# Performance work log

Measured on AMD Instinct MI355X. Metric: run time of the kernel, lower is better.

Reference implementation:

```python
import jax, jax.numpy as jnp
import numpy as np

B, SEQ, S, DIM_IN, DIM_K, DIM_V = 4, 2048, 128, 512, 64, 64
L = SEQ + 2 * S
NEG = -1e30  # stand-in for log(0) in the tril mask (finite for stable vjp)


def _layernorm(x, g, b, eps=1e-5):
    m = jnp.mean(x, axis=-1, keepdims=True)
    v = jnp.var(x, axis=-1, keepdims=True)
    return (x - m) / jnp.sqrt(v + eps) * g + b


def setup_inputs() -> dict:
    key = jax.random.key(0)
    ks = jax.random.split(key, 18)
    w = lambda k, shape, s=0.02: (jax.random.normal(k, shape, jnp.float32) * s)
    inp = {
        "x": jax.random.normal(ks[0], (B, L, DIM_IN), jnp.float32),
        "Wq": w(ks[1], (DIM_IN, DIM_K)),
        "Wk": w(ks[2], (DIM_IN, DIM_K)),
        "Wv": w(ks[3], (DIM_IN, DIM_V)),
        "Wq_s": w(ks[4], (DIM_IN, DIM_K)),
        "Wk_s": w(ks[5], (DIM_IN, DIM_K)),
        "Wv_s": w(ks[6], (DIM_IN, DIM_V)),
        "Wq_e": w(ks[7], (DIM_IN, DIM_K)),
        "Wk_e": w(ks[8], (DIM_IN, DIM_K)),
        "Wv_e": w(ks[9], (DIM_IN, DIM_V)),
        "ln_g": jnp.ones((DIM_IN,), jnp.float32),
        "ln_b": jnp.zeros((DIM_IN,), jnp.float32),
        "ln_s_g": jnp.ones((DIM_IN,), jnp.float32),
        "ln_s_b": jnp.zeros((DIM_IN,), jnp.float32),
        "ln_e_g": jnp.ones((DIM_IN,), jnp.float32),
        "ln_e_b": jnp.zeros((DIM_IN,), jnp.float32),
        "cope_emb": jax.random.normal(ks[10], (DIM_K, S), jnp.float32),
        "offset": 0,
    }
    return inp


def reference(x, Wq, Wk, Wv, Wq_s, Wk_s, Wv_s, Wq_e, Wk_e, Wv_e,
              ln_g, ln_b, ln_s_g, ln_s_b, ln_e_g, ln_e_b, cope_emb, offset):
    # extract_state: first/last state_len tokens
    xs, xm, xe = x[:, :S], x[:, S:L - S], x[:, -S:]
    xm = _layernorm(xm, ln_g, ln_b)
    xs = _layernorm(xs, ln_s_g, ln_s_b)
    xe = _layernorm(xe, ln_e_g, ln_e_b)

    q, k, v = xm @ Wq, xm @ Wk, xm @ Wv          # (B, SEQ, dk/dv)
    q_s, k_s, v_s = xs @ Wq_s, xs @ Wk_s, xs @ Wv_s
    q_e, k_e, v_e = xe @ Wq_e, xe @ Wk_e, xe @ Wv_e

    # CoPE bias over the non-state block
    logits = jnp.einsum('bqd,bkd->bqk', q, k)    # (B, SEQ, SEQ)
    gates = jax.nn.sigmoid(logits)
    pos = jnp.flip(jnp.cumsum(jnp.flip(gates, -1), axis=-1), -1)
    pos = jnp.minimum(pos, jnp.float32(S - 1))
    pos_ceil = jnp.ceil(pos).astype(jnp.int32)
    pos_floor = jnp.floor(pos).astype(jnp.int32)
    logits_int = jnp.einsum('bqd,dk->bqk', q, cope_emb)  # (B, SEQ, S)
    logits_c = jnp.take_along_axis(logits_int, pos_ceil, axis=-1)
    logits_f = jnp.take_along_axis(logits_int, pos_floor, axis=-1)
    wfrac = pos - pos_floor.astype(pos.dtype)
    bias = logits_c * wfrac + logits_f * (1.0 - wfrac)   # (B, SEQ, SEQ)

    q_full = jnp.concatenate([q_s, q, q_e], axis=1)      # (B, L, dk)
    k_full = jnp.concatenate([k_s, k, k_e], axis=1)
    v_full = jnp.concatenate([v_s, v, v_e], axis=1)

    # explicit tril log-mask bias with CoPE injected in the middle block
    tri = jnp.tril(jnp.ones((L, L), dtype=bool))
    attn_bias = jnp.where(tri, 0.0, NEG).astype(jnp.float32)
    attn_bias = jnp.broadcast_to(attn_bias, (B, L, L))
    attn_bias = attn_bias.at[:, S:L - S, S:L - S].add(bias)

    scale = 1.0 / jnp.sqrt(jnp.float32(DIM_K))
    scores = jnp.einsum('bqd,bkd->bqk', q_full, k_full) * scale + attn_bias
    att = jax.nn.softmax(scores, axis=-1)
    return jnp.einsum('bqk,bkd->bqd', att, v_full)       # (B, L, dv)
```

## Files before the change

kernel.cpp:

```cpp
#include <hip/hip_runtime.h>
#include <math.h>

#define B_    4
#define SEQ_  2048
#define S_    128
#define L_    2304
#define DIN   512
#define DK    64
#define NEGINF (-1e30f)
#define SCALE 0.125f
#define NCOLS 2176
#define NMID  8192
#define NEDGE 1024
#define LE    2304

typedef _Float16 f16;
typedef __attribute__((ext_vector_type(8))) _Float16 half8;
typedef __attribute__((ext_vector_type(4))) float f32x4;

union U4 { uint4 u; f16 h[8]; };

__global__ __launch_bounds__(256) void k_wsplit(
    const float* __restrict__ Wq,  const float* __restrict__ Wk,  const float* __restrict__ Wv,
    const float* __restrict__ Wqs, const float* __restrict__ Wks, const float* __restrict__ Wvs,
    const float* __restrict__ Wqe, const float* __restrict__ Wke, const float* __restrict__ Wve,
    f16* __restrict__ Wsp)
{
    __shared__ float xs[64 * 68];
    const int kt  = blockIdx.x;
    const int mat = blockIdx.y;
    const float* W;
    switch (mat) {
        case 0: W = Wq;  break; case 1: W = Wk;  break; case 2: W = Wv;  break;
        case 3: W = Wqs; break; case 4: W = Wks; break; case 5: W = Wvs; break;
        case 6: W = Wqe; break; case 7: W = Wke; break; default: W = Wve; break;
    }
    const int tid = threadIdx.x;
    const int k0  = kt * 64;
    #pragma unroll
    for (int i = 0; i < 4; ++i) {
        int g = tid + 256 * i;
        int k = g >> 4, c4 = g & 15;
        *(float4*)(xs + k * 68 + c4 * 4) = ((const float4*)W)[(size_t)(k0 + k) * 16 + c4];
    }
    __syncthreads();
    const int col = tid & 63, hf = tid >> 6;
    const int kk0 = hf * 16;
    U4 hi0, hi1, lo0, lo1;
    #pragma unroll
    for (int j = 0; j < 8; ++j) {
        float v0 = xs[(kk0 + j) * 68 + col];
        float v1 = xs[(kk0 + 8 + j) * 68 + col];
        hi0.h[j] = (f16)v0; lo0.h[j] = (f16)(v0 - (float)hi0.h[j]);
        hi1.h[j] = (f16)v1; lo1.h[j] = (f16)(v1 - (float)hi1.h[j]);
    }
    f16* dst = Wsp + (size_t)mat * 65536 + (size_t)col * 1024 + k0 + kk0;
    *(uint4*)(dst)       = hi0.u;
    *(uint4*)(dst + 8)   = hi1.u;
    *(uint4*)(dst + 512) = lo0.u;
    *(uint4*)(dst + 520) = lo1.u;
}

__global__ __launch_bounds__(256) void k_proj(
    const float* __restrict__ x, const f16* __restrict__ Wsp,
    const float* __restrict__ g0, const float* __restrict__ b0,
    const float* __restrict__ gs, const float* __restrict__ bs,
    const float* __restrict__ ge, const float* __restrict__ be,
    f16* __restrict__ qsp, f16* __restrict__ ksp, f16* __restrict__ vhT)
{
    __shared__ f16 As[32 * 136];
    __shared__ f16 Bs[3 * 64 * 136];
    __shared__ float mean_s[32], rstd_s[32];
    const int tid  = threadIdx.x;
    const int row0 = blockIdx.x * 32;
    const int rseq = row0 % L_;
    const int seg  = (rseq < S_) ? 0 : (rseq >= L_ - S_) ? 2 : 1;
    const int mat0 = (seg == 0) ? 3 : (seg == 2) ? 6 : 0;
    const float* gg = (seg == 0) ? gs : (seg == 2) ? ge : g0;
    const float* bb = (seg == 0) ? bs : (seg == 2) ? be : b0;

    {
        const int rr = tid >> 3, qq = tid & 7;
        const float4* xr = (const float4*)(x + (size_t)(row0 + rr) * DIN) + qq * 16;
        float s = 0.f, s2 = 0.f;
        #pragma unroll
        for (int i = 0; i < 16; ++i) {
            float4 v = xr[i];
            s  += v.x + v.y + v.z + v.w;
            s2 += v.x * v.x + v.y * v.y + v.z * v.z + v.w * v.w;
        }
        s  += __shfl_xor(s, 1);  s  += __shfl_xor(s, 2);  s  += __shfl_xor(s, 4);
        s2 += __shfl_xor(s2, 1); s2 += __shfl_xor(s2, 2); s2 += __shfl_xor(s2, 4);
        if (qq == 0) {
            float mean = s * (1.f / DIN);
            mean_s[rr] = mean;
            rstd_s[rr] = rsqrtf(s2 * (1.f / DIN) - mean * mean + 1e-5f);
        }
    }

    const int w = tid >> 6, lane = tid & 63;
    const int cl = lane & 15, quad = lane >> 4;
    const int r0 = 16 * (w >> 1), c0 = 32 * (w & 1);

    f32x4 acc[3][2];
    #pragma unroll
    for (int m = 0; m < 3; ++m)
        #pragma unroll
        for (int j = 0; j < 2; ++j) acc[m][j] = 0.f;

    for (int kc = 0; kc < DIN; kc += 64) {
        __syncthreads();
        {
            int r = tid >> 3, c8 = tid & 7;
            const float* xp = x + (size_t)(row0 + r) * DIN + kc + c8 * 8;
            float4 a0 = *(const float4*)xp;
            float4 a1 = *(const float4*)(xp + 4);
            float4 gA = *(const float4*)(gg + kc + c8 * 8);
            float4 gB = *(const float4*)(gg + kc + c8 * 8 + 4);
            float4 bA = *(const float4*)(bb + kc + c8 * 8);
            float4 bB = *(const float4*)(bb + kc + c8 * 8 + 4);
            float mean = mean_s[r], rstd = rstd_s[r];
            float n[8];
            n[0] = (a0.x - mean) * rstd * gA.x + bA.x;
            n[1] = (a0.y - mean) * rstd * gA.y + bA.y;
            n[2] = (a0.z - mean) * rstd * gA.z + bA.z;
            n[3] = (a0.w - mean) * rstd * gA.w + bA.w;
            n[4] = (a1.x - mean) * rstd * gB.x + bB.x;
            n[5] = (a1.y - mean) * rstd * gB.y + bB.y;
            n[6] = (a1.z - mean) * rstd * gB.z + bB.z;
            n[7] = (a1.w - mean) * rstd * gB.w + bB.w;
            U4 hi, lo;
            #pragma unroll
            for (int j = 0; j < 8; ++j) {
                hi.h[j] = (f16)n[j];
                lo.h[j] = (f16)(n[j] - (float)hi.h[j]);
            }
            *(uint4*)(As + r * 136 + c8 * 8)      = hi.u;
            *(uint4*)(As + r * 136 + 64 + c8 * 8) = lo.u;
        }
        #pragma unroll
        for (int i = 0; i < 6; ++i) {
            int g = tid + 256 * i;
            int mm = g >> 9, rem = g & 511;
            int col = rem >> 3, c8 = rem & 7;
            const f16* src = Wsp + (size_t)(mat0 + mm) * 65536 + (size_t)col * 1024 + kc + c8 * 8;
            f16* dst = Bs + mm * 8704 + col * 136 + c8 * 8;
            *(uint4*)(dst)      = *(const uint4*)(src);
            *(uint4*)(dst + 64) = *(const uint4*)(src + 512);
        }
        __syncthreads();
        #pragma unroll
        for (int h = 0; h < 2; ++h) {
            half8 ah, al;
            {
                const f16* base = As + (r0 + cl) * 136 + h * 32 + quad * 8;
                ah = *(const half8*)(base);
                al = *(const half8*)(base + 64);
            }
            #pragma unroll
            for (int m = 0; m < 3; ++m)
                #pragma unroll
                for (int cs = 0; cs < 2; ++cs) {
                    const f16* base = Bs + m * 8704 + (c0 + 16 * cs + cl) * 136 + h * 32 + quad * 8;
                    half8 bh = *(const half8*)(base);
                    half8 bl = *(const half8*)(base + 64);
                    acc[m][cs] = __builtin_amdgcn_mfma_f32_16x16x32_f16(ah, bh, acc[m][cs], 0, 0, 0);
                    acc[m][cs] = __builtin_amdgcn_mfma_f32_16x16x32_f16(ah, bl, acc[m][cs], 0, 0, 0);
                    acc[m][cs] = __builtin_amdgcn_mfma_f32_16x16x32_f16(al, bh, acc[m][cs], 0, 0, 0);
                }
        }
    }

    const int bI = row0 / L_;
    const int rb = row0 - bI * L_;
    #pragma unroll
    for (int m = 0; m < 3; ++m) {
        f16* sp = (m == 0) ? qsp : ksp;
        #pragma unroll
        for (int cs = 0; cs < 2; ++cs)
            #pragma unroll
            for (int r = 0; r < 4; ++r) {
                int lrow = r0 + quad * 4 + r;
                int col  = c0 + 16 * cs + cl;
                float v  = acc[m][cs][r];
                size_t grow = (size_t)(row0 + lrow);
                if (m < 2) {
                    f16 hv = (f16)v;
                    sp[grow * 128 + col]      = hv;
                    sp[grow * 128 + 64 + col] = (f16)(v - (float)hv);
                } else {
                    vhT[(size_t)(bI * 64 + col) * L_ + rb + lrow] = (f16)v;
                }
            }
    }
}

__global__ __launch_bounds__(256) void k_dots(
    const f16* __restrict__ qsp, const f16* __restrict__ ksp,
    float* __restrict__ D32, float* __restrict__ G, float* __restrict__ De32)
{
    const int bx = blockIdx.x, by = blockIdx.y;
    const bool edge = (bx >= 64);
    int b, q0 = 0;
    size_t qrow0;
    if (!edge) {
        if (by >= 17) return;
        b = bx >> 4;
        q0 = (bx * 128) & 2047;
        qrow0 = (size_t)b * L_ + S_ + q0;
    } else {
        int ex = bx - 64;
        b = ex >> 1;
        int half = ex & 1;
        if (half == 0 && by > 0) return;
        qrow0 = (size_t)b * L_ + (half ? 2176 : 0);
    }
    const int col0 = by * 128;
    const size_t krow0 = (size_t)b * L_ + col0;

    __shared__ f16 Qs[128 * 136];
    __shared__ f16 Ks[128 * 136];
    const int tid = threadIdx.x;

    #pragma unroll
    for (int i = 0; i < 8; ++i) {
        int g = tid + 256 * i;
        int r = g >> 4, c = g & 15;
        *(uint4*)(Qs + r * 136 + c * 8) = *(const uint4*)(qsp + (qrow0 + r) * 128 + c * 8);
        *(uint4*)(Ks + r * 136 + c * 8) = *(const uint4*)(ksp + (krow0 + r) * 128 + c * 8);
    }
    __syncthreads();

    const int w = tid >> 6, lane = tid & 63;
    const int cl = lane & 15, quad = lane >> 4;

    f32x4 acc[2][8];
    #pragma unroll
    for (int i = 0; i < 2; ++i)
        #pragma unroll
        for (int j = 0; j < 8; ++j) acc[i][j] = 0.f;

    #pragma unroll
    for (int h = 0; h < 2; ++h) {
        half8 ah[2], al[2];
        #pragma unroll
        for (int rs = 0; rs < 2; ++rs) {
            const f16* base = Qs + (32 * w + 16 * rs + cl) * 136 + h * 32 + quad * 8;
            ah[rs] = *(const half8*)(base);
            al[rs] = *(const half8*)(base + 64);
        }
        #pragma unroll
        for (int cq = 0; cq < 2; ++cq) {
            half8 bh[4], bl[4];
            #pragma unroll
            for (int cc = 0; cc < 4; ++cc) {
                const f16* base = Ks + (16 * (cq * 4 + cc) + cl) * 136 + h * 32 + quad * 8;
                bh[cc] = *(const half8*)(base);
                bl[cc] = *(const half8*)(base + 64);
            }
            #pragma unroll
            for (int rs = 0; rs < 2; ++rs)
                #pragma unroll
                for (int cc = 0; cc < 4; ++cc) {
                    int c = cq * 4 + cc;
                    acc[rs][c] = __builtin_amdgcn_mfma_f32_16x16x32_f16(ah[rs], bh[cc], acc[rs][c], 0, 0, 0);
                    acc[rs][c] = __builtin_amdgcn_mfma_f32_16x16x32_f16(ah[rs], bl[cc], acc[rs][c], 0, 0, 0);
                    acc[rs][c] = __builtin_amdgcn_mfma_f32_16x16x32_f16(al[rs], bh[cc], acc[rs][c], 0, 0, 0);
                }
        }
    }

    if (!edge) {
        const int gr0 = bx * 128;
        const bool writeD = (by == 0) || ((by - 1) <= (q0 >> 7));
        if (writeD) {
            #pragma unroll
            for (int rs = 0; rs < 2; ++rs)
                #pragma unroll
                for (int c = 0; c < 8; ++c)
                    #pragma unroll
                    for (int r = 0; r < 4; ++r) {
                        int mrow = gr0 + 32 * w + 16 * rs + quad * 4 + r;
                        int n    = col0 + 16 * c + cl;
                        D32[(size_t)mrow * NCOLS + n] = acc[rs][c][r];
                    }
        }
        if (by >= 1) {
            const int chm = 2 * (by - 1);
            #pragma unroll
            for (int rs = 0; rs < 2; ++rs)
                #pragma unroll
                for (int r = 0; r < 4; ++r) {
                    float sA = 0.f, sB = 0.f;
                    #pragma unroll
                    for (int cc = 0; cc < 4; ++cc) {
                        sA += 1.f / (1.f + __expf(-acc[rs][cc][r]));
                        sB += 1.f / (1.f + __expf(-acc[rs][4 + cc][r]));
                    }
                    #pragma unroll
                    for (int off = 1; off < 16; off <<= 1) {
                        sA += __shfl_xor(sA, off);
                        sB += __shfl_xor(sB, off);
                    }
                    if (cl == 0) {
                        int row = gr0 + 32 * w + 16 * rs + quad * 4 + r;
                        G[(size_t)row * 32 + chm]     = sA;
                        G[(size_t)row * 32 + chm + 1] = sB;
                    }
                }
        }
    } else {
        const int er0 = (bx - 64) * 128;
        #pragma unroll
        for (int rs = 0; rs < 2; ++rs)
            #pragma unroll
            for (int c = 0; c < 8; ++c)
                #pragma unroll
                for (int r = 0; r < 4; ++r) {
                    int erow = er0 + 32 * w + 16 * rs + quad * 4 + r;
                    int n    = col0 + 16 * c + cl;
                    De32[(size_t)erow * LE + n] = acc[rs][c][r];
                }
    }
}

__global__ __launch_bounds__(256) void k_scan(
    const f16* __restrict__ qsp, const float* __restrict__ cope,
    const float* __restrict__ G,
    const float* __restrict__ D32, f16* __restrict__ Dp,
    const float* __restrict__ De32, f16* __restrict__ Dep)
{
    __shared__ f16   qvh[128];
    __shared__ float li[128];
    __shared__ float Gs[32];
    __shared__ float Gsf[32];
    __shared__ float wmax[4], wsum[4];
    const int tid = threadIdx.x;
    const int gr  = blockIdx.x;
    const int lane = tid & 63, wid = tid >> 6;

    if (gr < NMID) {
        const int b = gr >> 11;
        const int q = gr & 2047;
        const size_t grow = (size_t)b * L_ + S_ + q;
        const int qlim = (q & ~63) + 64;

        if (tid < 16) ((uint4*)qvh)[tid] = ((const uint4*)(qsp + grow * 128))[tid];
        if (tid >= 16 && tid < 24)
            ((float4*)Gs)[tid - 16] = ((const float4*)G)[(size_t)gr * 8 + tid - 16];
        __syncthreads();
        if (tid < 128) {
            float a = 0.f;
            #pragma unroll
            for (int d = 0; d < DK; ++d)
                a += ((float)qvh[d] + (float)qvh[64 + d]) * cope[d * S_ + tid];
            li[tid] = a;
        }
        if (tid >= 128 && tid < 160) {
            int c = tid - 128;
            float s = 0.f;
            for (int cc = c + 1; cc < 32; ++cc) s += Gs[cc];
            Gsf[c] = s;
        }

        const float* Sr = D32 + (size_t)gr * NCOLS;
        f16* Dr = Dp + (size_t)gr * NCOLS;
        const int j0 = tid * 8;
        const int cg = tid >> 3, sl = tid & 7;
        float dot[8], gte[8];
        float csum = 0.f;
        if (j0 < qlim) {
            float4 t0 = *(const float4*)(Sr + 128 + j0);
            float4 t1 = *(const float4*)(Sr + 128 + j0 + 4);
            dot[0] = t0.x; dot[1] = t0.y; dot[2] = t0.z; dot[3] = t0.w;
            dot[4] = t1.x; dot[5] = t1.y; dot[6] = t1.z; dot[7] = t1.w;
            #pragma unroll
            for (int jj = 0; jj < 8; ++jj) {
                gte[jj] = 1.f / (1.f + __expf(-dot[jj]));
                csum += gte[jj];
            }
        } else {
            #pragma unroll
            for (int jj = 0; jj < 8; ++jj) { dot[jj] = 0.f; gte[jj] = 0.f; }
        }
        float sv = (tid < 128) ? Sr[tid] * SCALE : NEGINF;

        float inc = csum;
        #pragma unroll
        for (int off = 1; off < 8; off <<= 1) {
            float u = __shfl_down(inc, off, 8);
            if (sl + off < 8) inc += u;
        }
        __syncthreads();
        float run = (inc - csum) + Gsf[cg];

        float p8[8];
        #pragma unroll
        for (int jj = 7; jj >= 0; --jj) {
            run += gte[jj];
            float pos = fminf(run, (float)(S_ - 1));
            float pfl = floorf(pos);
            int ic  = (int)ceilf(pos);
            int ifl = (int)pfl;
            float w = pos - pfl;
            float bias = li[ic] * w + li[ifl] * (1.f - w);
            p8[jj] = (j0 + jj <= q) ? dot[jj] * SCALE + bias : NEGINF;
        }

        float mx = sv;
        #pragma unroll
        for (int jj = 0; jj < 8; ++jj) mx = fmaxf(mx, p8[jj]);
        #pragma unroll
        for (int off = 1; off < 64; off <<= 1) mx = fmaxf(mx, __shfl_xor(mx, off));
        if (lane == 0) wmax[wid] = mx;
        __syncthreads();
        mx = fmaxf(fmaxf(wmax[0], wmax[1]), fmaxf(wmax[2], wmax[3]));

        float lsum = 0.f;
        float e8[8];
        #pragma unroll
        for (int jj = 0; jj < 8; ++jj) {
            e8[jj] = __expf(p8[jj] - mx);
            lsum += e8[jj];
        }
        float es = 0.f;
        if (tid < 128) { es = __expf(sv - mx); lsum += es; }
        #pragma unroll
        for (int off = 1; off < 64; off <<= 1) lsum += __shfl_xor(lsum, off);
        if (lane == 0) wsum[wid] = lsum;
        __syncthreads();
        float inv = 1.f / (wsum[0] + wsum[1] + wsum[2] + wsum[3]);

        if (j0 < qlim) {
            U4 o;
            #pragma unroll
            for (int jj = 0; jj < 8; ++jj) o.h[jj] = (f16)(e8[jj] * inv);
            *(uint4*)(Dr + 128 + j0) = o.u;
        }
        if (tid < 128) Dr[tid] = (f16)(es * inv);
    } else {
        const int er = gr - NMID;
        const int r  = er & 255;
        const int Q  = (r < 128) ? r : (2048 + r);
        const float* Er32 = De32 + (size_t)er * LE;
        f16* Er = Dep + (size_t)er * LE;

        float v[9];
        #pragma unroll
        for (int i = 0; i < 9; ++i) {
            int j = tid + 256 * i;
            float d = Er32[j];
            v[i] = (j <= Q) ? d * SCALE : NEGINF;
        }
        float mx = v[0];
        #pragma unroll
        for (int i = 1; i < 9; ++i) mx = fmaxf(mx, v[i]);
        #pragma unroll
        for (int off = 1; off < 64; off <<= 1) mx = fmaxf(mx, __shfl_xor(mx, off));
        if (lane == 0) wmax[wid] = mx;
        __syncthreads();
        mx = fmaxf(fmaxf(wmax[0], wmax[1]), fmaxf(wmax[2], wmax[3]));

        float lsum = 0.f;
        #pragma unroll
        for (int i = 0; i < 9; ++i) {
            v[i] = __expf(v[i] - mx);
            lsum += v[i];
        }
        #pragma unroll
        for (int off = 1; off < 64; off <<= 1) lsum += __shfl_xor(lsum, off);
        if (lane == 0) wsum[wid] = lsum;
        __syncthreads();
        float inv = 1.f / (wsum[0] + wsum[1] + wsum[2] + wsum[3]);

        #pragma unroll
        for (int i = 0; i < 9; ++i)
            Er[tid + 256 * i] = (f16)(v[i] * inv);
    }
}

__global__ __launch_bounds__(256) void k_pv(
    const f16* __restrict__ Pmid, const f16* __restrict__ Pedge,
    const f16* __restrict__ vhT,
    float* __restrict__ Opart, float* __restrict__ Oe)
{
    __shared__ f16 Ps[64 * 72];
    __shared__ f16 Vt[64 * 72];
    const int tid = threadIdx.x;
    const int bx  = blockIdx.x;
    const int ks  = blockIdx.y;
    const bool edge = (bx >= 128);

    const f16* Pb;
    size_t pitch;
    int row0, b, cap, cmax;
    float* outp;
    if (!edge) {
        row0 = bx * 64;
        b = row0 >> 11;
        int q0 = row0 & 2047;
        Pb = Pmid; pitch = NCOLS; cap = 34;
        cmax = (191 + q0) >> 6;
        outp = Opart + (size_t)ks * NMID * DK;
    } else {
        row0 = (bx - 128) * 64;
        b = row0 >> 8;
        int r0 = row0 & 255;
        Pb = Pedge; pitch = LE; cap = 36;
        int Qmax = (r0 < 128) ? (r0 + 63) : (2048 + r0 + 63);
        cmax = Qmax >> 6;
        outp = Oe + (size_t)ks * NEDGE * DK;
    }
    const int c_beg = ks * 9;
    int c_end = c_beg + 9;
    if (c_end > cap) c_end = cap;
    if (c_end > cmax + 1) c_end = cmax + 1;

    const int w = tid >> 6, lane = tid & 63;
    const int cl = lane & 15, quad = lane >> 4;
    f32x4 acc[4];
    #pragma unroll
    for (int c = 0; c < 4; ++c) acc[c] = 0.f;

    for (int ch = c_beg; ch < c_end; ++ch) {
        __syncthreads();
        #pragma unroll
        for (int i = 0; i < 2; ++i) {
            int g = tid + 256 * i;
            int r = g >> 3, c = g & 7;
            *(uint4*)(Ps + r * 72 + c * 8) =
                *(const uint4*)(Pb + (size_t)(row0 + r) * pitch + ch * 64 + c * 8);
            *(uint4*)(Vt + r * 72 + c * 8) =
                *(const uint4*)(vhT + (size_t)(b * 64 + r) * L_ + ch * 64 + c * 8);
        }
        __syncthreads();
        #pragma unroll
        for (int h = 0; h < 2; ++h) {
            half8 a = *(const half8*)(Ps + (16 * w + cl) * 72 + h * 32 + quad * 8);
            #pragma unroll
            for (int c = 0; c < 4; ++c) {
                half8 bv = *(const half8*)(Vt + (16 * c + cl) * 72 + h * 32 + quad * 8);
                acc[c] = __builtin_amdgcn_mfma_f32_16x16x32_f16(a, bv, acc[c], 0, 0, 0);
            }
        }
    }
    #pragma unroll
    for (int c = 0; c < 4; ++c)
        #pragma unroll
        for (int r = 0; r < 4; ++r) {
            int mrow = row0 + 16 * w + quad * 4 + r;
            int n    = 16 * c + cl;
            outp[(size_t)mrow * DK + n] = acc[c][r];
        }
}

__global__ __launch_bounds__(256) void k_merge(
    const float* __restrict__ Opart, const float* __restrict__ Oe,
    float* __restrict__ out)
{
    const int e = blockIdx.x * 256 + threadIdx.x;
    if (e < NMID * DK) {
        const int gr = e >> 6, c = e & 63;
        const int b  = gr >> 11, q = gr & 2047;
        const int NP = NMID * DK;
        float s = Opart[e] + Opart[e + NP] + Opart[e + 2 * NP] + Opart[e + 3 * NP];
        out[((size_t)b * L_ + S_ + q) * DK + c] = s;
    } else {
        const int e2 = e - NMID * DK;
        const int er = e2 >> 6, c = e2 & 63;
        const int b  = er >> 8, r = er & 255;
        const int gQ = (r < 128) ? r : (2048 + r);
        const int NP = NEDGE * DK;
        float s = Oe[e2] + Oe[e2 + NP] + Oe[e2 + 2 * NP] + Oe[e2 + 3 * NP];
        out[((size_t)b * L_ + gQ) * DK + c] = s;
    }
}

extern "C" void kernel_launch(void* const* d_in, const int* in_sizes, int n_in,
                              void* d_out, int out_size, void* d_ws, size_t ws_size,
                              hipStream_t stream)
{
    const float* x    = (const float*)d_in[0];
    const float* Wq   = (const float*)d_in[1];
    const float* Wk   = (const float*)d_in[2];
    const float* Wv   = (const float*)d_in[3];
    const float* Wqs  = (const float*)d_in[4];
    const float* Wks  = (const float*)d_in[5];
    const float* Wvs  = (const float*)d_in[6];
    const float* Wqe  = (const float*)d_in[7];
    const float* Wke  = (const float*)d_in[8];
    const float* Wve  = (const float*)d_in[9];
    const float* g0   = (const float*)d_in[10];
    const float* b0   = (const float*)d_in[11];
    const float* gs   = (const float*)d_in[12];
    const float* bs   = (const float*)d_in[13];
    const float* ge   = (const float*)d_in[14];
    const float* be   = (const float*)d_in[15];
    const float* cope = (const float*)d_in[16];

    const size_t NR = (size_t)B_ * L_;
    f16*   qsp   = (f16*)d_ws;
    f16*   ksp   = qsp + NR * 128;
    f16*   vhT   = ksp + NR * 128;
    f16*   Wsp   = vhT + NR * 64;
    float* G     = (float*)(Wsp + (size_t)9 * 65536);
    float* Opart = G + (size_t)NMID * 32;
    float* Oe    = Opart + (size_t)4 * NMID * DK;
    float* Dm32  = Oe + (size_t)4 * NEDGE * DK;
    float* De32  = Dm32 + (size_t)NMID * NCOLS;
    f16*   Dp    = (f16*)(De32 + (size_t)NEDGE * LE);
    f16*   Dep   = Dp + (size_t)NMID * NCOLS;
    float* out   = (float*)d_out;

    k_wsplit<<<dim3(8, 9), 256, 0, stream>>>(Wq, Wk, Wv, Wqs, Wks, Wvs,
                                             Wqe, Wke, Wve, Wsp);
    k_proj<<<288, 256, 0, stream>>>(x, Wsp, g0, b0, gs, bs, ge, be,
                                    qsp, ksp, vhT);
    k_dots<<<dim3(72, 18), 256, 0, stream>>>(qsp, ksp, Dm32, G, De32);
    k_scan<<<NMID + NEDGE, 256, 0, stream>>>(qsp, cope, G, Dm32, Dp, De32, Dep);
    k_pv  <<<dim3(144, 4), 256, 0, stream>>>(Dp, Dep, vhT, Opart, Oe);
    k_merge<<<(NMID + NEDGE) * DK / 256, 256, 0, stream>>>(Opart, Oe, out);
}
```

Before: 194.6 us.

## Fuse PV split-K reduction into block, load Q and A fragments directly to registers

k_pv now runs 512-thread blocks over 32 rows. Four wave groups split the key chunks and reduce their partial results through shared memory before writing the final output, which removes the Opart/Oe buffers and the k_merge launch. k_proj and k_dots load the LayerNorm'd A operand and the Q fragments straight from global memory into MFMA registers instead of staging them in LDS, and k_dots gets a launch_bounds occupancy hint of 3. The trade-off is uncoalesced direct global loads and no LDS reuse of V across waves in k_pv.

```diff
diff --git a/kernel.cpp b/kernel.cpp
--- a/kernel.cpp
+++ b/kernel.cpp
@@ -18,7 +18,7 @@
 typedef __attribute__((ext_vector_type(8))) _Float16 half8;
 typedef __attribute__((ext_vector_type(4))) float f32x4;
 
-union U4 { uint4 u; f16 h[8]; };
+union U4 { uint4 u; f16 h[8]; half8 v; };
 
 __global__ __launch_bounds__(256) void k_wsplit(
     const float* __restrict__ Wq,  const float* __restrict__ Wk,  const float* __restrict__ Wv,
@@ -68,7 +68,6 @@
     const float* __restrict__ ge, const float* __restrict__ be,
     f16* __restrict__ qsp, f16* __restrict__ ksp, f16* __restrict__ vhT)
 {
-    __shared__ f16 As[32 * 136];
     __shared__ f16 Bs[3 * 64 * 136];
     __shared__ float mean_s[32], rstd_s[32];
     const int tid  = threadIdx.x;
@@ -108,18 +107,31 @@
         #pragma unroll
         for (int j = 0; j < 2; ++j) acc[m][j] = 0.f;
 
+    const int arow = row0 + r0 + cl;
+
     for (int kc = 0; kc < DIN; kc += 64) {
         __syncthreads();
-        {
-            int r = tid >> 3, c8 = tid & 7;
-            const float* xp = x + (size_t)(row0 + r) * DIN + kc + c8 * 8;
+        #pragma unroll
+        for (int i = 0; i < 6; ++i) {
+            int g = tid + 256 * i;
+            int mm = g >> 9, rem = g & 511;
+            int col = rem >> 3, c8 = rem & 7;
+            const f16* src = Wsp + (size_t)(mat0 + mm) * 65536 + (size_t)col * 1024 + kc + c8 * 8;
+            f16* dst = Bs + mm * 8704 + col * 136 + c8 * 8;
+            *(uint4*)(dst)      = *(const uint4*)(src);
+            *(uint4*)(dst + 64) = *(const uint4*)(src + 512);
+        }
+        __syncthreads();
+        const float mean = mean_s[r0 + cl], rstd = rstd_s[r0 + cl];
+        #pragma unroll
+        for (int h = 0; h < 2; ++h) {
+            const float* xp = x + (size_t)arow * DIN + kc + h * 32 + quad * 8;
             float4 a0 = *(const float4*)xp;
             float4 a1 = *(const float4*)(xp + 4);
-            float4 gA = *(const float4*)(gg + kc + c8 * 8);
-            float4 gB = *(const float4*)(gg + kc + c8 * 8 + 4);
-            float4 bA = *(const float4*)(bb + kc + c8 * 8);
-            float4 bB = *(const float4*)(bb + kc + c8 * 8 + 4);
-            float mean = mean_s[r], rstd = rstd_s[r];
+            const float* gp = gg + kc + h * 32 + quad * 8;
+            const float* bp = bb + kc + h * 32 + quad * 8;
+            float4 gA = *(const float4*)gp, gB = *(const float4*)(gp + 4);
+            float4 bA = *(const float4*)bp, bB = *(const float4*)(bp + 4);
             float n[8];
             n[0] = (a0.x - mean) * rstd * gA.x + bA.x;
             n[1] = (a0.y - mean) * rstd * gA.y + bA.y;
@@ -135,28 +147,7 @@
                 hi.h[j] = (f16)n[j];
                 lo.h[j] = (f16)(n[j] - (float)hi.h[j]);
             }
-            *(uint4*)(As + r * 136 + c8 * 8)      = hi.u;
-            *(uint4*)(As + r * 136 + 64 + c8 * 8) = lo.u;
-        }
-        #pragma unroll
-        for (int i = 0; i < 6; ++i) {
-            int g = tid + 256 * i;
-            int mm = g >> 9, rem = g & 511;
-            int col = rem >> 3, c8 = rem & 7;
-            const f16* src = Wsp + (size_t)(mat0 + mm) * 65536 + (size_t)col * 1024 + kc + c8 * 8;
-            f16* dst = Bs + mm * 8704 + col * 136 + c8 * 8;
-            *(uint4*)(dst)      = *(const uint4*)(src);
-            *(uint4*)(dst + 64) = *(const uint4*)(src + 512);
-        }
-        __syncthreads();
-        #pragma unroll
-        for (int h = 0; h < 2; ++h) {
-            half8 ah, al;
-            {
-                const f16* base = As + (r0 + cl) * 136 + h * 32 + quad * 8;
-                ah = *(const half8*)(base);
-                al = *(const half8*)(base + 64);
-            }
+            half8 ah = hi.v, al = lo.v;
             #pragma unroll
             for (int m = 0; m < 3; ++m)
                 #pragma unroll
@@ -195,7 +186,7 @@
     }
 }
 
-__global__ __launch_bounds__(256) void k_dots(
+__global__ __launch_bounds__(256, 3) void k_dots(
     const f16* __restrict__ qsp, const f16* __restrict__ ksp,
     float* __restrict__ D32, float* __restrict__ G, float* __restrict__ De32)
 {
@@ -218,22 +209,29 @@
     const int col0 = by * 128;
     const size_t krow0 = (size_t)b * L_ + col0;
 
-    __shared__ f16 Qs[128 * 136];
     __shared__ f16 Ks[128 * 136];
     const int tid = threadIdx.x;
+    const int w = tid >> 6, lane = tid & 63;
+    const int cl = lane & 15, quad = lane >> 4;
+
+    half8 qh[2][2], qlo[2][2];
+    #pragma unroll
+    for (int rs = 0; rs < 2; ++rs)
+        #pragma unroll
+        for (int h = 0; h < 2; ++h) {
+            const f16* qp = qsp + (qrow0 + 32 * w + 16 * rs + cl) * 128 + h * 32 + quad * 8;
+            qh[rs][h]  = *(const half8*)qp;
+            qlo[rs][h] = *(const half8*)(qp + 64);
+        }
 
     #pragma unroll
     for (int i = 0; i < 8; ++i) {
         int g = tid + 256 * i;
         int r = g >> 4, c = g & 15;
-        *(uint4*)(Qs + r * 136 + c * 8) = *(const uint4*)(qsp + (qrow0 + r) * 128 + c * 8);
         *(uint4*)(Ks + r * 136 + c * 8) = *(const uint4*)(ksp + (krow0 + r) * 128 + c * 8);
     }
     __syncthreads();
 
-    const int w = tid >> 6, lane = tid & 63;
-    const int cl = lane & 15, quad = lane >> 4;
-
     f32x4 acc[2][8];
     #pragma unroll
     for (int i = 0; i < 2; ++i)
@@ -242,13 +240,6 @@
 
     #pragma unroll
     for (int h = 0; h < 2; ++h) {
-        half8 ah[2], al[2];
-        #pragma unroll
-        for (int rs = 0; rs < 2; ++rs) {
-            const f16* base = Qs + (32 * w + 16 * rs + cl) * 136 + h * 32 + quad * 8;
-            ah[rs] = *(const half8*)(base);
-            al[rs] = *(const half8*)(base + 64);
-        }
         #pragma unroll
         for (int cq = 0; cq < 2; ++cq) {
             half8 bh[4], bl[4];
@@ -263,9 +254,9 @@
                 #pragma unroll
                 for (int cc = 0; cc < 4; ++cc) {
                     int c = cq * 4 + cc;
-                    acc[rs][c] = __builtin_amdgcn_mfma_f32_16x16x32_f16(ah[rs], bh[cc], acc[rs][c], 0, 0, 0);
-                    acc[rs][c] = __builtin_amdgcn_mfma_f32_16x16x32_f16(ah[rs], bl[cc], acc[rs][c], 0, 0, 0);
-                    acc[rs][c] = __builtin_amdgcn_mfma_f32_16x16x32_f16(al[rs], bh[cc], acc[rs][c], 0, 0, 0);
+                    acc[rs][c] = __builtin_amdgcn_mfma_f32_16x16x32_f16(qh[rs][h], bh[cc], acc[rs][c], 0, 0, 0);
+                    acc[rs][c] = __builtin_amdgcn_mfma_f32_16x16x32_f16(qh[rs][h], bl[cc], acc[rs][c], 0, 0, 0);
+                    acc[rs][c] = __builtin_amdgcn_mfma_f32_16x16x32_f16(qlo[rs][h], bh[cc], acc[rs][c], 0, 0, 0);
                 }
         }
     }
@@ -479,100 +470,77 @@
     }
 }
 
-__global__ __launch_bounds__(256) void k_pv(
+__global__ __launch_bounds__(512) void k_pv(
     const f16* __restrict__ Pmid, const f16* __restrict__ Pedge,
-    const f16* __restrict__ vhT,
-    float* __restrict__ Opart, float* __restrict__ Oe)
+    const f16* __restrict__ vhT, float* __restrict__ out)
 {
-    __shared__ f16 Ps[64 * 72];
-    __shared__ f16 Vt[64 * 72];
-    const int tid = threadIdx.x;
-    const int bx  = blockIdx.x;
-    const int ks  = blockIdx.y;
-    const bool edge = (bx >= 128);
-
-    const f16* Pb;
-    size_t pitch;
-    int row0, b, cap, cmax;
-    float* outp;
-    if (!edge) {
-        row0 = bx * 64;
-        b = row0 >> 11;
-        int q0 = row0 & 2047;
-        Pb = Pmid; pitch = NCOLS; cap = 34;
-        cmax = (191 + q0) >> 6;
-        outp = Opart + (size_t)ks * NMID * DK;
-    } else {
-        row0 = (bx - 128) * 64;
-        b = row0 >> 8;
-        int r0 = row0 & 255;
-        Pb = Pedge; pitch = LE; cap = 36;
-        int Qmax = (r0 < 128) ? (r0 + 63) : (2048 + r0 + 63);
-        cmax = Qmax >> 6;
-        outp = Oe + (size_t)ks * NEDGE * DK;
-    }
-    const int c_beg = ks * 9;
-    int c_end = c_beg + 9;
-    if (c_end > cap) c_end = cap;
-    if (c_end > cmax + 1) c_end = cmax + 1;
-
+    __shared__ float mbuf[3][2][16 * 68];
+    const int tid = threadIdx.x, bx = blockIdx.x;
     const int w = tid >> 6, lane = tid & 63;
     const int cl = lane & 15, quad = lane >> 4;
+    const int g = w >> 2, ql = w & 3;
+    const bool edge = (bx >= 256);
+
+    const f16* Pb;
+    size_t prow0, pitch;
+    int b, cmax, cap, q0 = 0, r0 = 0;
+    if (!edge) {
+        int gr0 = bx * 32;
+        b = gr0 >> 11; q0 = gr0 & 2047;
+        Pb = Pmid; prow0 = gr0; pitch = NCOLS; cap = 34;
+        cmax = (159 + q0) >> 6;
+    } else {
+        int er0 = (bx - 256) * 32;
+        b = er0 >> 8; r0 = er0 & 255;
+        Pb = Pedge; prow0 = er0; pitch = LE; cap = 36;
+        int Qmax = (r0 < 128) ? (r0 + 31) : (2048 + r0 + 31);
+        cmax = Qmax >> 6;
+    }
+    int c_end = cmax + 1;
+    if (c_end > cap) c_end = cap;
+
     f32x4 acc[4];
     #pragma unroll
     for (int c = 0; c < 4; ++c) acc[c] = 0.f;
 
-    for (int ch = c_beg; ch < c_end; ++ch) {
-        __syncthreads();
-        #pragma unroll
-        for (int i = 0; i < 2; ++i) {
-            int g = tid + 256 * i;
-            int r = g >> 3, c = g & 7;
-            *(uint4*)(Ps + r * 72 + c * 8) =
-                *(const uint4*)(Pb + (size_t)(row0 + r) * pitch + ch * 64 + c * 8);
-            *(uint4*)(Vt + r * 72 + c * 8) =
-                *(const uint4*)(vhT + (size_t)(b * 64 + r) * L_ + ch * 64 + c * 8);
-        }
-        __syncthreads();
+    for (int ch = ql; ch < c_end; ch += 4) {
         #pragma unroll
         for (int h = 0; h < 2; ++h) {
-            half8 a = *(const half8*)(Ps + (16 * w + cl) * 72 + h * 32 + quad * 8);
-            #pragma unroll
-            for (int c = 0; c < 4; ++c) {
-                half8 bv = *(const half8*)(Vt + (16 * c + cl) * 72 + h * 32 + quad * 8);
-                acc[c] = __builtin_amdgcn_mfma_f32_16x16x32_f16(a, bv, acc[c], 0, 0, 0);
+            half8 pa = *(const half8*)(Pb + (prow0 + 16 * g + cl) * pitch + ch * 64 + h * 32 + quad * 8);
+            #pragma unroll
+            for (int c2 = 0; c2 < 4; ++c2) {
+                half8 bv = *(const half8*)(vhT + (size_t)(b * 64 + 16 * c2 + cl) * L_ + ch * 64 + h * 32 + quad * 8);
+                acc[c2] = __builtin_amdgcn_mfma_f32_16x16x32_f16(pa, bv, acc[c2], 0, 0, 0);
             }
         }
     }
-    #pragma unroll
-    for (int c = 0; c < 4; ++c)
-        #pragma unroll
-        for (int r = 0; r < 4; ++r) {
-            int mrow = row0 + 16 * w + quad * 4 + r;
-            int n    = 16 * c + cl;
-            outp[(size_t)mrow * DK + n] = acc[c][r];
-        }
-}
-
-__global__ __launch_bounds__(256) void k_merge(
-    const float* __restrict__ Opart, const float* __restrict__ Oe,
-    float* __restrict__ out)
-{
-    const int e = blockIdx.x * 256 + threadIdx.x;
-    if (e < NMID * DK) {
-        const int gr = e >> 6, c = e & 63;
-        const int b  = gr >> 11, q = gr & 2047;
-        const int NP = NMID * DK;
-        float s = Opart[e] + Opart[e + NP] + Opart[e + 2 * NP] + Opart[e + 3 * NP];
-        out[((size_t)b * L_ + S_ + q) * DK + c] = s;
-    } else {
-        const int e2 = e - NMID * DK;
-        const int er = e2 >> 6, c = e2 & 63;
-        const int b  = er >> 8, r = er & 255;
-        const int gQ = (r < 128) ? r : (2048 + r);
-        const int NP = NEDGE * DK;
-        float s = Oe[e2] + Oe[e2 + NP] + Oe[e2 + 2 * NP] + Oe[e2 + 3 * NP];
-        out[((size_t)b * L_ + gQ) * DK + c] = s;
+
+    if (ql != 0) {
+        #pragma unroll
+        for (int c2 = 0; c2 < 4; ++c2)
+            #pragma unroll
+            for (int r = 0; r < 4; ++r)
+                mbuf[ql - 1][g][(quad * 4 + r) * 68 + 16 * c2 + cl] = acc[c2][r];
+    }
+    __syncthreads();
+    if (ql == 0) {
+        #pragma unroll
+        for (int c2 = 0; c2 < 4; ++c2)
+            #pragma unroll
+            for (int r = 0; r < 4; ++r) {
+                int idx = (quad * 4 + r) * 68 + 16 * c2 + cl;
+                float v = acc[c2][r] + mbuf[0][g][idx] + mbuf[1][g][idx] + mbuf[2][g][idx];
+                int lrow = 16 * g + quad * 4 + r;
+                size_t grow;
+                if (!edge) {
+                    grow = (size_t)b * L_ + S_ + q0 + lrow;
+                } else {
+                    int rr = r0 + lrow;
+                    int gQ = (rr < 128) ? rr : (2048 + rr);
+                    grow = (size_t)b * L_ + gQ;
+                }
+                out[grow * DK + 16 * c2 + cl] = v;
+            }
     }
 }
 
@@ -604,9 +572,7 @@
     f16*   vhT   = ksp + NR * 128;
     f16*   Wsp   = vhT + NR * 64;
     float* G     = (float*)(Wsp + (size_t)9 * 65536);
-    float* Opart = G + (size_t)NMID * 32;
-    float* Oe    = Opart + (size_t)4 * NMID * DK;
-    float* Dm32  = Oe + (size_t)4 * NEDGE * DK;
+    float* Dm32  = G + (size_t)NMID * 32;
     float* De32  = Dm32 + (size_t)NMID * NCOLS;
     f16*   Dp    = (f16*)(De32 + (size_t)NEDGE * LE);
     f16*   Dep   = Dp + (size_t)NMID * NCOLS;
@@ -618,6 +584,5 @@
                                     qsp, ksp, vhT);
     k_dots<<<dim3(72, 18), 256, 0, stream>>>(qsp, ksp, Dm32, G, De32);
     k_scan<<<NMID + NEDGE, 256, 0, stream>>>(qsp, cope, G, Dm32, Dp, De32, Dep);
-    k_pv  <<<dim3(144, 4), 256, 0, stream>>>(Dp, Dep, vhT, Opart, Oe);
-    k_merge<<<(NMID + NEDGE) * DK / 256, 256, 0, stream>>>(Opart, Oe, out);
+    k_pv<<<288, 512, 0, stream>>>(Dp, Dep, vhT, out);
 }
```

Measured after the change: 229.1 us. 17.7% more time.
